# Optimization experiments

Measured on AMD Instinct MI355X. Metric: run time of the kernel, lower is better.

## Reference

```python
import jax, jax.numpy as jnp
import numpy as np

N = 100000
E = 1600000
IN = 256
H = 4
D = 32           # n_hidden per head
C = 47           # n_classes per head in last layer
NEG_SLOPE = 0.2


def setup_inputs() -> dict:
    key = jax.random.key(0)
    ks = jax.random.split(key, 20)
    x = jax.random.normal(ks[0], (N, IN), dtype=jnp.float32)
    src = jax.random.randint(ks[1], (E,), 0, N, dtype=jnp.int32)
    dst = jax.random.randint(ks[2], (E,), 0, N, dtype=jnp.int32)
    s = 0.05
    inp = {"x": x, "src": src, "dst": dst}
    # layer 0: in 256 -> (H=4, D=32)
    inp["W0s"] = jax.random.normal(ks[3], (IN, H * D), dtype=jnp.float32) * s
    inp["W0d"] = jax.random.normal(ks[4], (IN, H * D), dtype=jnp.float32) * s
    inp["a0l"] = jax.random.normal(ks[5], (H, D), dtype=jnp.float32) * s
    inp["a0r"] = jax.random.normal(ks[6], (H, D), dtype=jnp.float32) * s
    inp["b0"] = jnp.zeros((H, D), dtype=jnp.float32)
    # layer 1: in 128 -> (4, 32)
    inp["W1s"] = jax.random.normal(ks[7], (H * D, H * D), dtype=jnp.float32) * s
    inp["W1d"] = jax.random.normal(ks[8], (H * D, H * D), dtype=jnp.float32) * s
    inp["a1l"] = jax.random.normal(ks[9], (H, D), dtype=jnp.float32) * s
    inp["a1r"] = jax.random.normal(ks[10], (H, D), dtype=jnp.float32) * s
    inp["b1"] = jnp.zeros((H, D), dtype=jnp.float32)
    # layer 2: in 128 -> (4, 47), no activation
    inp["W2s"] = jax.random.normal(ks[11], (H * D, H * C), dtype=jnp.float32) * s
    inp["W2d"] = jax.random.normal(ks[12], (H * D, H * C), dtype=jnp.float32) * s
    inp["a2l"] = jax.random.normal(ks[13], (H, C), dtype=jnp.float32) * s
    inp["a2r"] = jax.random.normal(ks[14], (H, C), dtype=jnp.float32) * s
    inp["b2"] = jnp.zeros((H, C), dtype=jnp.float32)
    return inp


def _gat_layer(h, src, dst, Ws, Wd, al, ar, b):
    # h: [N, F_in]; full-graph block so h_dst == h
    n = h.shape[0]
    heads, dout = al.shape
    fs = (h @ Ws).reshape(n, heads, dout)   # [N, H, D]
    fd = (h @ Wd).reshape(n, heads, dout)
    el = jnp.sum(fs * al, axis=-1)          # [N, H]
    er = jnp.sum(fd * ar, axis=-1)
    e = el[src] + er[dst]                   # [E, H]
    e = jnp.where(e > 0, e, NEG_SLOPE * e)  # leaky_relu
    # segment softmax over incoming edges of each dst node
    m = jax.lax.stop_gradient(jax.ops.segment_max(e, dst, num_segments=n))
    ez = jnp.exp(e - m[dst])
    denom = jax.ops.segment_sum(ez, dst, num_segments=n)
    alpha = ez / denom[dst]                 # [E, H]
    msg = fs[src] * alpha[:, :, None]       # [E, H, D]
    rst = jax.ops.segment_sum(msg, dst, num_segments=n)  # [N, H, D]
    return rst + b


def reference(x, src, dst,
              W0s, W0d, a0l, a0r, b0,
              W1s, W1d, a1l, a1r, b1,
              W2s, W2d, a2l, a2r, b2):
    h = _gat_layer(x, src, dst, W0s, W0d, a0l, a0r, b0)
    h = jax.nn.relu(h).reshape(h.shape[0], -1)           # flatten(1)
    h = _gat_layer(h, src, dst, W1s, W1d, a1l, a1r, b1)
    h = jax.nn.relu(h).reshape(h.shape[0], -1)
    h = _gat_layer(h, src, dst, W2s, W2d, a2l, a2r, b2)  # [N, H, C]
    h = h.mean(axis=1)                                   # mean over heads
    return jax.nn.log_softmax(h, axis=-1)
```

## Files before the change

kernel.cpp:

```cpp
#include <hip/hip_runtime.h>
#include <math.h>

#define NEG_SLOPE 0.2f

typedef _Float16 half2v __attribute__((ext_vector_type(2)));
typedef _Float16 half8 __attribute__((ext_vector_type(8)));
typedef float float4v __attribute__((ext_vector_type(4)));
typedef float float2v __attribute__((ext_vector_type(2)));

__device__ __forceinline__ float lrelu(float x) { return x > 0.f ? x : NEG_SLOPE * x; }

__device__ __forceinline__ float sel4(const float4 v, int h) {
  float r = v.x;
  r = (h == 1) ? v.y : r;
  r = (h == 2) ? v.z : r;
  r = (h == 3) ? v.w : r;
  return r;
}

__device__ __forceinline__ unsigned char f32_to_fp8(float a) {
  int v = __builtin_amdgcn_cvt_pk_fp8_f32(a, 0.f, 0, false);
  return (unsigned char)(v & 0xff);
}

__device__ __forceinline__ void acc16(float2v acc[8], uint4 d, float ez) {
  float2v ez2 = {ez, ez};
  float2v c;
  c = __builtin_amdgcn_cvt_pk_f32_fp8((int)d.x, false); acc[0] += ez2 * c;
  c = __builtin_amdgcn_cvt_pk_f32_fp8((int)d.x, true);  acc[1] += ez2 * c;
  c = __builtin_amdgcn_cvt_pk_f32_fp8((int)d.y, false); acc[2] += ez2 * c;
  c = __builtin_amdgcn_cvt_pk_f32_fp8((int)d.y, true);  acc[3] += ez2 * c;
  c = __builtin_amdgcn_cvt_pk_f32_fp8((int)d.z, false); acc[4] += ez2 * c;
  c = __builtin_amdgcn_cvt_pk_f32_fp8((int)d.z, true);  acc[5] += ez2 * c;
  c = __builtin_amdgcn_cvt_pk_f32_fp8((int)d.w, false); acc[6] += ez2 * c;
  c = __builtin_amdgcn_cvt_pk_f32_fp8((int)d.w, true);  acc[7] += ez2 * c;
}


__global__ void k_hist(const int* __restrict__ dst, int* __restrict__ cnt, int E) {
  int i = blockIdx.x * blockDim.x + threadIdx.x;
  if (i < E) atomicAdd(&cnt[dst[i]], 1);
}

__global__ __launch_bounds__(256) void k_offsets(const int* __restrict__ cnt,
                                                 int* __restrict__ row_start,
                                                 int* __restrict__ gcount, int N) {
  __shared__ int s[256];
  __shared__ int base;
  int tid = threadIdx.x;
  int i = blockIdx.x * 256 + tid;
  int c = (i < N) ? cnt[i] : 0;
  s[tid] = c;
  __syncthreads();
  for (int off = 1; off < 256; off <<= 1) {
    int v = 0;
    if (tid >= off) v = s[tid - off];
    __syncthreads();
    if (tid >= off) s[tid] += v;
    __syncthreads();
  }
  if (tid == 255) base = atomicAdd(gcount, s[255]);
  __syncthreads();
  if (i < N) row_start[i] = base + s[tid] - c;
}

__global__ void k_scatter(const int* __restrict__ src, const int* __restrict__ dst,
                          const int* __restrict__ row_start, int* __restrict__ fill,
                          int* __restrict__ srcs, int E) {
  int i = blockIdx.x * blockDim.x + threadIdx.x;
  if (i < E) {
    int d = dst[i];
    int p = row_start[d] + atomicAdd(&fill[d], 1);
    srcs[p] = src[i];
  }
}

__device__ __forceinline__ void wlr_one(const float* Ws, const float* Wd,
                                        const float* al, const float* ar,
                                        float* wlr, int K, int Dh, int i) {
  int M = 4 * Dh;
  int k = i >> 2, h = i & 3;
  float sl = 0.f, sr = 0.f;
  for (int d = 0; d < Dh; d++) {
    sl += Ws[(size_t)k * M + h * Dh + d] * al[h * Dh + d];
    sr += Wd[(size_t)k * M + h * Dh + d] * ar[h * Dh + d];
  }
  wlr[k * 8 + h] = sl;
  wlr[k * 8 + 4 + h] = sr;
}

__global__ __launch_bounds__(256) void k_prep(
    const float* __restrict__ W0s, const float* __restrict__ W0d,
    const float* __restrict__ a0l, const float* __restrict__ a0r,
    const float* __restrict__ W1s, const float* __restrict__ W1d,
    const float* __restrict__ a1l, const float* __restrict__ a1r,
    const float* __restrict__ W2s, const float* __restrict__ W2d,
    const float* __restrict__ a2l, const float* __restrict__ a2r,
    float* __restrict__ wlr0, float* __restrict__ wlr1, float* __restrict__ wlr2,
    _Float16* __restrict__ Wt0, _Float16* __restrict__ Wt1, _Float16* __restrict__ Wt2) {
  int i = blockIdx.x * 256 + threadIdx.x;
  if (i < 1024) {
    wlr_one(W0s, W0d, a0l, a0r, wlr0, 256, 32, i);
  } else if (i < 1536) {
    wlr_one(W1s, W1d, a1l, a1r, wlr1, 128, 32, i - 1024);
  } else if (i < 2048) {
    wlr_one(W2s, W2d, a2l, a2r, wlr2, 128, 47, i - 1536);
  } else if (i < 2048 + 32768) {
    int j = i - 2048;
    int m = j >> 8, k = j & 255;
    Wt0[j] = (_Float16)W0s[(size_t)k * 128 + m];
  } else if (i < 2048 + 32768 + 16384) {
    int j = i - (2048 + 32768);
    int m = j >> 7, k = j & 127;
    Wt1[j] = (_Float16)W1s[(size_t)k * 128 + m];
  } else if (i < 2048 + 32768 + 16384 + 24576) {
    int j = i - (2048 + 32768 + 16384);
    int r = j >> 7, k = j & 127;
    int h = r / 48, c = r % 48;
    float v = (c < 47) ? W2s[(size_t)k * 188 + 47 * h + c] : 0.f;
    Wt2[j] = (_Float16)v;
  }
}

template <int BN, typename AT>
__global__ __launch_bounds__(256) void k_gemm_mfma(const AT* __restrict__ A,
                                                   const _Float16* __restrict__ Bt,
                                                   const float* __restrict__ wlr,
                                                   unsigned char* __restrict__ C,
                                                   float* __restrict__ el,
                                                   float* __restrict__ er, int N, int K) {
  constexpr int NT = BN / 64;
  constexpr int ASZ = 4 * 64 * 8;
  constexpr int BSZ = (BN / 16) * 64 * 8;
  constexpr int SSZ = ASZ + BSZ;
  __shared__ __align__(16) _Float16 smem[SSZ];
  __shared__ float swlr[2048];
  _Float16* As = smem;
  _Float16* Bs = smem + ASZ;

  const int tid = threadIdx.x;
  const int lane = tid & 63;
  const int w = tid >> 6;
  const int row0 = blockIdx.x * 64;

  for (int i = tid; i < K * 8; i += 256) swlr[i] = wlr[i];
  __syncthreads();

  float4v acc[4][NT];
#pragma unroll
  for (int i = 0; i < 4; i++)
#pragma unroll
    for (int j = 0; j < NT; j++) acc[i][j] = (float4v){0.f, 0.f, 0.f, 0.f};
  float p[8] = {0, 0, 0, 0, 0, 0, 0, 0};

  const int ar_ = tid >> 2, aq = tid & 3;
  for (int k0 = 0; k0 < K; k0 += 32) {
    {
      int gr = row0 + ar_;
      float a8[8];
      if (gr < N) {
        if constexpr (sizeof(AT) == 4) {
          const float4* pp = (const float4*)&A[(size_t)gr * K + k0 + aq * 8];
          float4 u0 = pp[0], u1 = pp[1];
          a8[0] = u0.x; a8[1] = u0.y; a8[2] = u0.z; a8[3] = u0.w;
          a8[4] = u1.x; a8[5] = u1.y; a8[6] = u1.z; a8[7] = u1.w;
        } else {
          half8 hv = *(const half8*)&A[(size_t)gr * K + k0 + aq * 8];
#pragma unroll
          for (int j = 0; j < 8; j++) a8[j] = (float)hv[j];
        }
      } else {
#pragma unroll
        for (int j = 0; j < 8; j++) a8[j] = 0.f;
      }
      half8 v;
#pragma unroll
      for (int j = 0; j < 8; j++) v[j] = (_Float16)a8[j];
      *(half8*)&As[(size_t)(((ar_ >> 4) * 64) + (ar_ & 15) + 16 * aq) * 8] = v;
#pragma unroll
      for (int j = 0; j < 8; j++) {
        const float av = a8[j];
        const float* wp = &swlr[(k0 + aq * 8 + j) * 8];
        float4 w0 = *(const float4*)wp;
        float4 w1 = *(const float4*)(wp + 4);
        p[0] += av * w0.x; p[1] += av * w0.y; p[2] += av * w0.z; p[3] += av * w0.w;
        p[4] += av * w1.x; p[5] += av * w1.y; p[6] += av * w1.z; p[7] += av * w1.w;
      }
    }
#pragma unroll
    for (int i = 0; i < NT; i++) {
      int idx = tid + i * 256;
      int n = idx >> 2, q = idx & 3;
      half8 v = *(const half8*)&Bt[(size_t)n * K + k0 + q * 8];
      *(half8*)&Bs[(size_t)((n >> 4) * 64 + (n & 15) + 16 * q) * 8] = v;
    }
    __syncthreads();
    half8 af[4];
#pragma unroll
    for (int mt = 0; mt < 4; mt++) af[mt] = *(half8*)&As[(size_t)(mt * 64 + lane) * 8];
#pragma unroll
    for (int nt = 0; nt < NT; nt++) {
      half8 bf = *(half8*)&Bs[(size_t)((w * NT + nt) * 64 + lane) * 8];
#pragma unroll
      for (int mt = 0; mt < 4; mt++)
        acc[mt][nt] = __builtin_amdgcn_mfma_f32_16x16x32_f16(af[mt], bf, acc[mt][nt], 0, 0, 0);
    }
    __syncthreads();
  }

#pragma unroll
  for (int j = 0; j < 8; j++) swlr[(ar_ * 4 + aq) * 8 + j] = p[j];

  unsigned char* cs = (unsigned char*)smem;
  const int quad = lane >> 4;
#pragma unroll
  for (int mt = 0; mt < 4; mt++)
#pragma unroll
    for (int nt = 0; nt < NT; nt++)
#pragma unroll
      for (int reg = 0; reg < 4; reg++) {
        int r = mt * 16 + quad * 4 + reg;
        int cc = (w * NT + nt) * 16 + (lane & 15);
        cs[r * BN + cc] = f32_to_fp8(acc[mt][nt][reg]);
      }
  __syncthreads();
  if (tid < 64) {
    int gr = row0 + tid;
    if (gr < N) {
      float e[8];
#pragma unroll
      for (int j = 0; j < 8; j++)
        e[j] = swlr[(tid * 4 + 0) * 8 + j] + swlr[(tid * 4 + 1) * 8 + j] +
               swlr[(tid * 4 + 2) * 8 + j] + swlr[(tid * 4 + 3) * 8 + j];
      *(float4*)&el[(size_t)gr * 4] = make_float4(e[0], e[1], e[2], e[3]);
      *(float4*)&er[(size_t)gr * 4] = make_float4(e[4], e[5], e[6], e[7]);
    }
  }
  constexpr int PER = (64 * BN) / (256 * 16);
  const uint4* s4 = (const uint4*)cs;
#pragma unroll
  for (int i = 0; i < PER; i++) {
    int idx = tid + i * 256;
    int r = idx / (BN / 16), c16 = idx % (BN / 16);
    int gr = row0 + r;
    if (gr < N) *(uint4*)&C[(size_t)gr * BN + c16 * 16] = s4[idx];
  }
}

__global__ __launch_bounds__(256) void k_edge_mid(
    const unsigned char* __restrict__ F, const float* __restrict__ el,
    const float* __restrict__ er, const int* __restrict__ row_start,
    const int* __restrict__ cnt, const int* __restrict__ srcs,
    const float* __restrict__ bias, _Float16* __restrict__ hout, int N) {
  __shared__ float sEz[4][64][4];
  __shared__ int sU[4][64];
  int lane = threadIdx.x & 63;
  int w = threadIdx.x >> 6;
  int v = blockIdx.x * 4 + w;
  if (v >= N) return;
  int start = row_start[v], deg = cnt[v];
  float4 erv = *(const float4*)&er[(size_t)v * 4];
  const int g8 = lane >> 3;
  const int sl = lane & 7;
  const int h = sl >> 1;
  float2v acc2[8];
#pragma unroll
  for (int i = 0; i < 8; i++) acc2[i] = (float2v){0.f, 0.f};
  float4 lsum = make_float4(0.f, 0.f, 0.f, 0.f);

  for (int c = 0; c < deg; c += 64) {
    int take = min(64, deg - c);
    if (lane < take) {
      int u = srcs[start + c + lane];
      float4 e = *(const float4*)&el[(size_t)u * 4];
      float4 ez;
      ez.x = __expf(lrelu(e.x + erv.x));
      ez.y = __expf(lrelu(e.y + erv.y));
      ez.z = __expf(lrelu(e.z + erv.z));
      ez.w = __expf(lrelu(e.w + erv.w));
      lsum.x += ez.x; lsum.y += ez.y; lsum.z += ez.z; lsum.w += ez.w;
      sU[w][lane] = u;
      *(float4*)&sEz[w][lane][0] = ez;
    }
    int kk = g8;
    if (kk < take) {
      int u0 = sU[w][kk];
      float ez0 = sEz[w][kk][h];
      uint4 d0 = *(const uint4*)&F[((unsigned)u0 << 7) + 16u * (unsigned)sl];
      for (kk += 8; kk < take; kk += 8) {
        int u1 = sU[w][kk];
        float ez1 = sEz[w][kk][h];
        uint4 d1 = *(const uint4*)&F[((unsigned)u1 << 7) + 16u * (unsigned)sl];
        acc16(acc2, d0, ez0);
        d0 = d1; ez0 = ez1;
      }
      acc16(acc2, d0, ez0);
    }
  }
#pragma unroll
  for (int m = 8; m < 64; m <<= 1)
#pragma unroll
    for (int i = 0; i < 8; i++) {
      acc2[i].x += __shfl_xor(acc2[i].x, m);
      acc2[i].y += __shfl_xor(acc2[i].y, m);
    }
#pragma unroll
  for (int msk = 1; msk < 64; msk <<= 1) {
    lsum.x += __shfl_xor(lsum.x, msk);
    lsum.y += __shfl_xor(lsum.y, msk);
    lsum.z += __shfl_xor(lsum.z, msk);
    lsum.w += __shfl_xor(lsum.w, msk);
  }
  if (g8 == 0) {
    float inv = (deg > 0) ? 1.f / sel4(lsum, h) : 0.f;
    const float4* bp = (const float4*)&bias[16 * sl];
    float4 b0v = bp[0], b1v = bp[1], b2v = bp[2], b3v = bp[3];
    float bb[16] = {b0v.x, b0v.y, b0v.z, b0v.w, b1v.x, b1v.y, b1v.z, b1v.w,
                    b2v.x, b2v.y, b2v.z, b2v.w, b3v.x, b3v.y, b3v.z, b3v.w};
    half8 o0, o1;
#pragma unroll
    for (int j = 0; j < 8; j++) {
      float a = acc2[j >> 1][j & 1];
      o0[j] = (_Float16)fmaxf(fmaf(a, inv, bb[j]), 0.f);
    }
#pragma unroll
    for (int j = 0; j < 8; j++) {
      float a = acc2[(j + 8) >> 1][j & 1];
      o1[j] = (_Float16)fmaxf(fmaf(a, inv, bb[j + 8]), 0.f);
    }
    *(half8*)&hout[(size_t)v * 128 + 16 * sl] = o0;
    *(half8*)&hout[(size_t)v * 128 + 16 * sl + 8] = o1;
  }
}

__global__ __launch_bounds__(256) void k_edge_final(
    const unsigned char* __restrict__ F, const float* __restrict__ el,
    const float* __restrict__ er, const int* __restrict__ row_start,
    const int* __restrict__ cnt, const int* __restrict__ srcs,
    const float* __restrict__ b2, float* __restrict__ out, int N) {
  __shared__ float sEz[4][64][4];
  __shared__ int sU[4][64];
  __shared__ float red[4][192];
  int lane = threadIdx.x & 63;
  int w = threadIdx.x >> 6;
  int v = blockIdx.x * 4 + w;
  if (v >= N) return;
  int start = row_start[v], deg = cnt[v];
  float4 erv = *(const float4*)&er[(size_t)v * 4];
  const int e0 = lane / 12;
  const int sl = lane - e0 * 12;
  const bool act = e0 < 5;
  const int h = sl / 3;
  float2v acc2[8];
#pragma unroll
  for (int i = 0; i < 8; i++) acc2[i] = (float2v){0.f, 0.f};
  float4 lsum = make_float4(0.f, 0.f, 0.f, 0.f);

  for (int c = 0; c < deg; c += 64) {
    int take = min(64, deg - c);
    if (lane < take) {
      int u = srcs[start + c + lane];
      float4 e = *(const float4*)&el[(size_t)u * 4];
      float4 ez;
      ez.x = __expf(lrelu(e.x + erv.x));
      ez.y = __expf(lrelu(e.y + erv.y));
      ez.z = __expf(lrelu(e.z + erv.z));
      ez.w = __expf(lrelu(e.w + erv.w));
      lsum.x += ez.x; lsum.y += ez.y; lsum.z += ez.z; lsum.w += ez.w;
      sU[w][lane] = u;
      *(float4*)&sEz[w][lane][0] = ez;
    }
    if (act) {
      int kk = e0;
      if (kk < take) {
        int u0 = sU[w][kk];
        float ez0 = sEz[w][kk][h];
        uint4 d0 = *(const uint4*)&F[(unsigned)u0 * 192u + 16u * (unsigned)sl];
        for (kk += 5; kk < take; kk += 5) {
          int u1 = sU[w][kk];
          float ez1 = sEz[w][kk][h];
          uint4 d1 = *(const uint4*)&F[(unsigned)u1 * 192u + 16u * (unsigned)sl];
          acc16(acc2, d0, ez0);
          d0 = d1; ez0 = ez1;
        }
        acc16(acc2, d0, ez0);
      }
    }
  }
#pragma unroll
  for (int i = 0; i < 8; i++) {
    float ax = acc2[i].x, ay = acc2[i].y;
    float t1x = ax + __shfl(ax, lane + 12);
    float t1y = ay + __shfl(ay, lane + 12);
    float t2x = t1x + __shfl(t1x, lane + 24);
    float t2y = t1y + __shfl(t1y, lane + 24);
    acc2[i].x = t2x + __shfl(ax, lane + 48);
    acc2[i].y = t2y + __shfl(ay, lane + 48);
  }
#pragma unroll
  for (int msk = 1; msk < 64; msk <<= 1) {
    lsum.x += __shfl_xor(lsum.x, msk);
    lsum.y += __shfl_xor(lsum.y, msk);
    lsum.z += __shfl_xor(lsum.z, msk);
    lsum.w += __shfl_xor(lsum.w, msk);
  }
  if (lane < 12) {
    float inv = (deg > 0) ? 1.f / sel4(lsum, h) : 0.f;
#pragma unroll
    for (int j = 0; j < 8; j++) {
      red[w][sl * 16 + 2 * j] = acc2[j].x * inv;
      red[w][sl * 16 + 2 * j + 1] = acc2[j].y * inv;
    }
  }
  float g = -INFINITY;
  if (lane < 47) {
    float s4 = red[w][lane] + red[w][lane + 48] + red[w][lane + 96] + red[w][lane + 144];
    float bsum = b2[lane] + b2[47 + lane] + b2[94 + lane] + b2[141 + lane];
    g = 0.25f * (s4 + bsum);
  }
  float gm = g;
#pragma unroll
  for (int msk = 1; msk < 64; msk <<= 1) gm = fmaxf(gm, __shfl_xor(gm, msk));
  float ex = (lane < 47) ? __expf(g - gm) : 0.f;
  float s = ex;
#pragma unroll
  for (int msk = 1; msk < 64; msk <<= 1) s += __shfl_xor(s, msk);
  if (lane < 47) out[(size_t)v * 47 + lane] = g - gm - __logf(s);
}

extern "C" void kernel_launch(void* const* d_in, const int* in_sizes, int n_in,
                              void* d_out, int out_size, void* d_ws, size_t ws_size,
                              hipStream_t stream) {
  const float* x = (const float*)d_in[0];
  const int* src = (const int*)d_in[1];
  const int* dst = (const int*)d_in[2];
  const float* W0s = (const float*)d_in[3];
  const float* W0d = (const float*)d_in[4];
  const float* a0l = (const float*)d_in[5];
  const float* a0r = (const float*)d_in[6];
  const float* b0 = (const float*)d_in[7];
  const float* W1s = (const float*)d_in[8];
  const float* W1d = (const float*)d_in[9];
  const float* a1l = (const float*)d_in[10];
  const float* a1r = (const float*)d_in[11];
  const float* b1 = (const float*)d_in[12];
  const float* W2s = (const float*)d_in[13];
  const float* W2d = (const float*)d_in[14];
  const float* a2l = (const float*)d_in[15];
  const float* a2r = (const float*)d_in[16];
  const float* b2 = (const float*)d_in[17];
  float* out = (float*)d_out;

  const int N = in_sizes[0] / 256;
  const int E = in_sizes[1];

  char* w = (char*)d_ws;
  size_t off = 0;
  auto alloc = [&](size_t bytes) -> void* {
    void* p = w + off;
    off += (bytes + 255) & ~(size_t)255;
    return p;
  };
  int* gcount = (int*)alloc(4);
  int* cnt = (int*)alloc((size_t)N * 4);
  int* fill = (int*)alloc((size_t)N * 4);
  size_t zbytes = off;
  int* row_start = (int*)alloc((size_t)N * 4);
  int* srcs = (int*)alloc((size_t)E * 4);
  float* wlr0 = (float*)alloc(256 * 8 * 4);
  float* wlr1 = (float*)alloc(128 * 8 * 4);
  float* wlr2 = (float*)alloc(128 * 8 * 4);
  _Float16* Wt0 = (_Float16*)alloc(128 * 256 * 2);
  _Float16* Wt1 = (_Float16*)alloc(128 * 128 * 2);
  _Float16* Wt2 = (_Float16*)alloc(192 * 128 * 2);
  float* el = (float*)alloc((size_t)N * 4 * 4);
  float* er = (float*)alloc((size_t)N * 4 * 4);
  unsigned char* F = (unsigned char*)alloc((size_t)N * 192);
  _Float16* Ha = (_Float16*)alloc((size_t)N * 128 * 2);
  _Float16* Hc = (_Float16*)alloc((size_t)N * 128 * 2);
  (void)ws_size;

  hipMemsetAsync(d_ws, 0, zbytes, stream);
  k_hist<<<(E + 255) / 256, 256, 0, stream>>>(dst, cnt, E);
  k_offsets<<<(N + 255) / 256, 256, 0, stream>>>(cnt, row_start, gcount, N);
  k_scatter<<<(E + 255) / 256, 256, 0, stream>>>(src, dst, row_start, fill, srcs, E);
  k_prep<<<(75776 + 255) / 256, 256, 0, stream>>>(W0s, W0d, a0l, a0r, W1s, W1d, a1l, a1r,
                                                  W2s, W2d, a2l, a2r, wlr0, wlr1, wlr2,
                                                  Wt0, Wt1, Wt2);

  int gemm_grid = (N + 63) / 64;
  int node_grid = (N + 3) / 4;

  k_gemm_mfma<128, float><<<gemm_grid, 256, 0, stream>>>(x, Wt0, wlr0, F, el, er, N, 256);
  k_edge_mid<<<node_grid, 256, 0, stream>>>(F, el, er, row_start, cnt, srcs, b0, Ha, N);

  k_gemm_mfma<128, _Float16><<<gemm_grid, 256, 0, stream>>>(Ha, Wt1, wlr1, F, el, er, N, 128);
  k_edge_mid<<<node_grid, 256, 0, stream>>>(F, el, er, row_start, cnt, srcs, b1, Hc, N);

  k_gemm_mfma<192, _Float16><<<gemm_grid, 256, 0, stream>>>(Hc, Wt2, wlr2, F, el, er, N, 128);
  k_edge_final<<<node_grid, 256, 0, stream>>>(F, el, er, row_start, cnt, srcs, b2, out, N);
}
```

Baseline: 712.8 us.

## Split edge aggregation across feature slices and separate final log-softmax combine

The edge aggregation kernels now split each node's feature row into slices handled by different blocks: two 64-byte halves for the middle layers and three slices for the final layer. Each lane covers fewer bytes, so 16 edges are processed in parallel instead of 8 or 5. Block indices are interleaved so that slices of nearby nodes run close together, which is meant to improve gather parallelism and keep the shared source rows in cache. The final layer writes per-slice partial results in fp16 to a scratch buffer, and a new combine kernel then does the head mean and log-softmax. In exchange, edge indices and attention exponentials are recomputed for every slice, and the extra kernel adds a launch and a scratch-buffer round trip.

```diff
diff --git a/kernel.cpp b/kernel.cpp
--- a/kernel.cpp
+++ b/kernel.cpp
@@ -247,22 +247,114 @@
   }
 }
 
-__global__ __launch_bounds__(256) void k_edge_mid(
+__global__ __launch_bounds__(256) void k_edge_mid_x(
     const unsigned char* __restrict__ F, const float* __restrict__ el,
     const float* __restrict__ er, const int* __restrict__ row_start,
     const int* __restrict__ cnt, const int* __restrict__ srcs,
     const float* __restrict__ bias, _Float16* __restrict__ hout, int N) {
+  __shared__ float sEz[4][64][2];
+  __shared__ int sU[4][64];
+  const int NB = (N + 3) >> 2;
+  const int p = blockIdx.x & 7;
+  const int s = p >> 2;
+  const int nb = (blockIdx.x >> 3) * 4 + (p & 3);
+  if (nb >= NB) return;
+  const int lane = threadIdx.x & 63;
+  const int w = threadIdx.x >> 6;
+  const int v = nb * 4 + w;
+  if (v >= N) return;
+  const int start = row_start[v], deg = cnt[v];
+  const float2 erv = *(const float2*)&er[(size_t)v * 4 + 2 * s];
+  const int g = lane >> 2;
+  const int sl = lane & 3;
+  const int hl = sl >> 1;
+  float2v acc2[8];
+#pragma unroll
+  for (int i = 0; i < 8; i++) acc2[i] = (float2v){0.f, 0.f};
+  float2 lsum = make_float2(0.f, 0.f);
+
+  for (int c = 0; c < deg; c += 64) {
+    int take = min(64, deg - c);
+    if (lane < take) {
+      int u = srcs[start + c + lane];
+      float2 e = *(const float2*)&el[(size_t)u * 4 + 2 * s];
+      float ezx = __expf(lrelu(e.x + erv.x));
+      float ezy = __expf(lrelu(e.y + erv.y));
+      lsum.x += ezx; lsum.y += ezy;
+      sU[w][lane] = u;
+      sEz[w][lane][0] = ezx;
+      sEz[w][lane][1] = ezy;
+    }
+    int kk = g;
+    if (kk < take) {
+      int u0 = sU[w][kk];
+      float ez0 = sEz[w][kk][hl];
+      uint4 d0 = *(const uint4*)&F[((unsigned)u0 << 7) + (unsigned)(s * 64 + sl * 16)];
+      for (kk += 16; kk < take; kk += 16) {
+        int u1 = sU[w][kk];
+        float ez1 = sEz[w][kk][hl];
+        uint4 d1 = *(const uint4*)&F[((unsigned)u1 << 7) + (unsigned)(s * 64 + sl * 16)];
+        acc16(acc2, d0, ez0);
+        d0 = d1; ez0 = ez1;
+      }
+      acc16(acc2, d0, ez0);
+    }
+  }
+#pragma unroll
+  for (int m = 4; m < 64; m <<= 1)
+#pragma unroll
+    for (int i = 0; i < 8; i++) {
+      acc2[i].x += __shfl_xor(acc2[i].x, m);
+      acc2[i].y += __shfl_xor(acc2[i].y, m);
+    }
+#pragma unroll
+  for (int msk = 1; msk < 64; msk <<= 1) {
+    lsum.x += __shfl_xor(lsum.x, msk);
+    lsum.y += __shfl_xor(lsum.y, msk);
+  }
+  if (g == 0) {
+    float inv = (deg > 0) ? 1.f / (hl ? lsum.y : lsum.x) : 0.f;
+    const int f0 = s * 64 + sl * 16;
+    const float4* bp = (const float4*)&bias[f0];
+    float4 b0v = bp[0], b1v = bp[1], b2v = bp[2], b3v = bp[3];
+    float bb[16] = {b0v.x, b0v.y, b0v.z, b0v.w, b1v.x, b1v.y, b1v.z, b1v.w,
+                    b2v.x, b2v.y, b2v.z, b2v.w, b3v.x, b3v.y, b3v.z, b3v.w};
+    half8 o0, o1;
+#pragma unroll
+    for (int j = 0; j < 8; j++)
+      o0[j] = (_Float16)fmaxf(fmaf(acc2[j >> 1][j & 1], inv, bb[j]), 0.f);
+#pragma unroll
+    for (int j = 0; j < 8; j++)
+      o1[j] = (_Float16)fmaxf(fmaf(acc2[(j + 8) >> 1][j & 1], inv, bb[j + 8]), 0.f);
+    *(half8*)&hout[(size_t)v * 128 + f0] = o0;
+    *(half8*)&hout[(size_t)v * 128 + f0 + 8] = o1;
+  }
+}
+
+__global__ __launch_bounds__(256) void k_edge_final_x(
+    const unsigned char* __restrict__ F, const float* __restrict__ el,
+    const float* __restrict__ er, const int* __restrict__ row_start,
+    const int* __restrict__ cnt, const int* __restrict__ srcs,
+    _Float16* __restrict__ Pf, int N) {
   __shared__ float sEz[4][64][4];
   __shared__ int sU[4][64];
-  int lane = threadIdx.x & 63;
-  int w = threadIdx.x >> 6;
-  int v = blockIdx.x * 4 + w;
+  const int NB = (N + 3) >> 2;
+  const int p = blockIdx.x & 7;
+  const int s = (p < 3) ? 0 : ((p < 6) ? 1 : 2);
+  const int r = p - 3 * s;
+  const int K = (s == 2) ? 2 : 3;
+  const int nb = (blockIdx.x >> 3) * K + r;
+  if (nb >= NB) return;
+  const int lane = threadIdx.x & 63;
+  const int w = threadIdx.x >> 6;
+  const int v = nb * 4 + w;
   if (v >= N) return;
-  int start = row_start[v], deg = cnt[v];
-  float4 erv = *(const float4*)&er[(size_t)v * 4];
-  const int g8 = lane >> 3;
-  const int sl = lane & 7;
-  const int h = sl >> 1;
+  const int start = row_start[v], deg = cnt[v];
+  const float4 erv = *(const float4*)&er[(size_t)v * 4];
+  const int g = lane >> 2;
+  const int sl = lane & 3;
+  const int k16 = 4 * s + sl;
+  const int h = k16 / 3;
   float2v acc2[8];
 #pragma unroll
   for (int i = 0; i < 8; i++) acc2[i] = (float2v){0.f, 0.f};
@@ -282,15 +374,15 @@
       sU[w][lane] = u;
       *(float4*)&sEz[w][lane][0] = ez;
     }
-    int kk = g8;
+    int kk = g;
     if (kk < take) {
       int u0 = sU[w][kk];
       float ez0 = sEz[w][kk][h];
-      uint4 d0 = *(const uint4*)&F[((unsigned)u0 << 7) + 16u * (unsigned)sl];
-      for (kk += 8; kk < take; kk += 8) {
+      uint4 d0 = *(const uint4*)&F[(unsigned)u0 * 192u + (unsigned)(k16 * 16)];
+      for (kk += 16; kk < take; kk += 16) {
         int u1 = sU[w][kk];
         float ez1 = sEz[w][kk][h];
-        uint4 d1 = *(const uint4*)&F[((unsigned)u1 << 7) + 16u * (unsigned)sl];
+        uint4 d1 = *(const uint4*)&F[(unsigned)u1 * 192u + (unsigned)(k16 * 16)];
         acc16(acc2, d0, ez0);
         d0 = d1; ez0 = ez1;
       }
@@ -298,7 +390,7 @@
     }
   }
 #pragma unroll
-  for (int m = 8; m < 64; m <<= 1)
+  for (int m = 4; m < 64; m <<= 1)
 #pragma unroll
     for (int i = 0; i < 8; i++) {
       acc2[i].x += __shfl_xor(acc2[i].x, m);
@@ -311,121 +403,41 @@
     lsum.z += __shfl_xor(lsum.z, msk);
     lsum.w += __shfl_xor(lsum.w, msk);
   }
-  if (g8 == 0) {
+  if (g == 0) {
     float inv = (deg > 0) ? 1.f / sel4(lsum, h) : 0.f;
-    const float4* bp = (const float4*)&bias[16 * sl];
-    float4 b0v = bp[0], b1v = bp[1], b2v = bp[2], b3v = bp[3];
-    float bb[16] = {b0v.x, b0v.y, b0v.z, b0v.w, b1v.x, b1v.y, b1v.z, b1v.w,
-                    b2v.x, b2v.y, b2v.z, b2v.w, b3v.x, b3v.y, b3v.z, b3v.w};
     half8 o0, o1;
 #pragma unroll
-    for (int j = 0; j < 8; j++) {
-      float a = acc2[j >> 1][j & 1];
-      o0[j] = (_Float16)fmaxf(fmaf(a, inv, bb[j]), 0.f);
-    }
-#pragma unroll
-    for (int j = 0; j < 8; j++) {
-      float a = acc2[(j + 8) >> 1][j & 1];
-      o1[j] = (_Float16)fmaxf(fmaf(a, inv, bb[j + 8]), 0.f);
-    }
-    *(half8*)&hout[(size_t)v * 128 + 16 * sl] = o0;
-    *(half8*)&hout[(size_t)v * 128 + 16 * sl + 8] = o1;
-  }
-}
-
-__global__ __launch_bounds__(256) void k_edge_final(
-    const unsigned char* __restrict__ F, const float* __restrict__ el,
-    const float* __restrict__ er, const int* __restrict__ row_start,
-    const int* __restrict__ cnt, const int* __restrict__ srcs,
-    const float* __restrict__ b2, float* __restrict__ out, int N) {
-  __shared__ float sEz[4][64][4];
-  __shared__ int sU[4][64];
-  __shared__ float red[4][192];
+    for (int j = 0; j < 8; j++) o0[j] = (_Float16)(acc2[j >> 1][j & 1] * inv);
+#pragma unroll
+    for (int j = 0; j < 8; j++) o1[j] = (_Float16)(acc2[(j + 8) >> 1][j & 1] * inv);
+    *(half8*)&Pf[(size_t)v * 192 + k16 * 16] = o0;
+    *(half8*)&Pf[(size_t)v * 192 + k16 * 16 + 8] = o1;
+  }
+}
+
+__global__ __launch_bounds__(256) void k_comb(const _Float16* __restrict__ Pf,
+                                              const float* __restrict__ b2,
+                                              float* __restrict__ out, int N) {
   int lane = threadIdx.x & 63;
   int w = threadIdx.x >> 6;
   int v = blockIdx.x * 4 + w;
   if (v >= N) return;
-  int start = row_start[v], deg = cnt[v];
-  float4 erv = *(const float4*)&er[(size_t)v * 4];
-  const int e0 = lane / 12;
-  const int sl = lane - e0 * 12;
-  const bool act = e0 < 5;
-  const int h = sl / 3;
-  float2v acc2[8];
-#pragma unroll
-  for (int i = 0; i < 8; i++) acc2[i] = (float2v){0.f, 0.f};
-  float4 lsum = make_float4(0.f, 0.f, 0.f, 0.f);
-
-  for (int c = 0; c < deg; c += 64) {
-    int take = min(64, deg - c);
-    if (lane < take) {
-      int u = srcs[start + c + lane];
-      float4 e = *(const float4*)&el[(size_t)u * 4];
-      float4 ez;
-      ez.x = __expf(lrelu(e.x + erv.x));
-      ez.y = __expf(lrelu(e.y + erv.y));
-      ez.z = __expf(lrelu(e.z + erv.z));
-      ez.w = __expf(lrelu(e.w + erv.w));
-      lsum.x += ez.x; lsum.y += ez.y; lsum.z += ez.z; lsum.w += ez.w;
-      sU[w][lane] = u;
-      *(float4*)&sEz[w][lane][0] = ez;
-    }
-    if (act) {
-      int kk = e0;
-      if (kk < take) {
-        int u0 = sU[w][kk];
-        float ez0 = sEz[w][kk][h];
-        uint4 d0 = *(const uint4*)&F[(unsigned)u0 * 192u + 16u * (unsigned)sl];
-        for (kk += 5; kk < take; kk += 5) {
-          int u1 = sU[w][kk];
-          float ez1 = sEz[w][kk][h];
-          uint4 d1 = *(const uint4*)&F[(unsigned)u1 * 192u + 16u * (unsigned)sl];
-          acc16(acc2, d0, ez0);
-          d0 = d1; ez0 = ez1;
-        }
-        acc16(acc2, d0, ez0);
-      }
-    }
-  }
-#pragma unroll
-  for (int i = 0; i < 8; i++) {
-    float ax = acc2[i].x, ay = acc2[i].y;
-    float t1x = ax + __shfl(ax, lane + 12);
-    float t1y = ay + __shfl(ay, lane + 12);
-    float t2x = t1x + __shfl(t1x, lane + 24);
-    float t2y = t1y + __shfl(t1y, lane + 24);
-    acc2[i].x = t2x + __shfl(ax, lane + 48);
-    acc2[i].y = t2y + __shfl(ay, lane + 48);
-  }
-#pragma unroll
-  for (int msk = 1; msk < 64; msk <<= 1) {
-    lsum.x += __shfl_xor(lsum.x, msk);
-    lsum.y += __shfl_xor(lsum.y, msk);
-    lsum.z += __shfl_xor(lsum.z, msk);
-    lsum.w += __shfl_xor(lsum.w, msk);
-  }
-  if (lane < 12) {
-    float inv = (deg > 0) ? 1.f / sel4(lsum, h) : 0.f;
-#pragma unroll
-    for (int j = 0; j < 8; j++) {
-      red[w][sl * 16 + 2 * j] = acc2[j].x * inv;
-      red[w][sl * 16 + 2 * j + 1] = acc2[j].y * inv;
-    }
-  }
-  float g = -INFINITY;
+  float gv = -INFINITY;
   if (lane < 47) {
-    float s4 = red[w][lane] + red[w][lane + 48] + red[w][lane + 96] + red[w][lane + 144];
-    float bsum = b2[lane] + b2[47 + lane] + b2[94 + lane] + b2[141 + lane];
-    g = 0.25f * (s4 + bsum);
-  }
-  float gm = g;
+    const _Float16* pr = &Pf[(size_t)v * 192];
+    float s4 = (float)pr[lane] + (float)pr[lane + 48] + (float)pr[lane + 96] +
+               (float)pr[lane + 144];
+    float bs = b2[lane] + b2[47 + lane] + b2[94 + lane] + b2[141 + lane];
+    gv = 0.25f * (s4 + bs);
+  }
+  float gm = gv;
 #pragma unroll
   for (int msk = 1; msk < 64; msk <<= 1) gm = fmaxf(gm, __shfl_xor(gm, msk));
-  float ex = (lane < 47) ? __expf(g - gm) : 0.f;
-  float s = ex;
-#pragma unroll
-  for (int msk = 1; msk < 64; msk <<= 1) s += __shfl_xor(s, msk);
-  if (lane < 47) out[(size_t)v * 47 + lane] = g - gm - __logf(s);
+  float ex = (lane < 47) ? __expf(gv - gm) : 0.f;
+  float ss = ex;
+#pragma unroll
+  for (int msk = 1; msk < 64; msk <<= 1) ss += __shfl_xor(ss, msk);
+  if (lane < 47) out[(size_t)v * 47 + lane] = gv - gm - __logf(ss);
 }
 
 extern "C" void kernel_launch(void* const* d_in, const int* in_sizes, int n_in,
@@ -478,6 +490,7 @@
   unsigned char* F = (unsigned char*)alloc((size_t)N * 192);
   _Float16* Ha = (_Float16*)alloc((size_t)N * 128 * 2);
   _Float16* Hc = (_Float16*)alloc((size_t)N * 128 * 2);
+  _Float16* Pf = Ha;
   (void)ws_size;
 
   hipMemsetAsync(d_ws, 0, zbytes, stream);
@@ -488,15 +501,18 @@
                                                   W2s, W2d, a2l, a2r, wlr0, wlr1, wlr2,
                                                   Wt0, Wt1, Wt2);
 
-  int gemm_grid = (N + 63) / 64;
-  int node_grid = (N + 3) / 4;
+  const int NB = (N + 3) / 4;
+  const int gemm_grid = (N + 63) / 64;
+  const int grid_mid = ((2 * NB + 7) / 8) * 8;
+  const int grid_fin = 8 * ((NB + 1) / 2);
 
   k_gemm_mfma<128, float><<<gemm_grid, 256, 0, stream>>>(x, Wt0, wlr0, F, el, er, N, 256);
-  k_edge_mid<<<node_grid, 256, 0, stream>>>(F, el, er, row_start, cnt, srcs, b0, Ha, N);
+  k_edge_mid_x<<<grid_mid, 256, 0, stream>>>(F, el, er, row_start, cnt, srcs, b0, Ha, N);
 
   k_gemm_mfma<128, _Float16><<<gemm_grid, 256, 0, stream>>>(Ha, Wt1, wlr1, F, el, er, N, 128);
-  k_edge_mid<<<node_grid, 256, 0, stream>>>(F, el, er, row_start, cnt, srcs, b1, Hc, N);
+  k_edge_mid_x<<<grid_mid, 256, 0, stream>>>(F, el, er, row_start, cnt, srcs, b1, Hc, N);
 
   k_gemm_mfma<192, _Float16><<<gemm_grid, 256, 0, stream>>>(Hc, Wt2, wlr2, F, el, er, N, 128);
-  k_edge_final<<<node_grid, 256, 0, stream>>>(F, el, er, row_start, cnt, srcs, b2, out, N);
-}
+  k_edge_final_x<<<grid_fin, 256, 0, stream>>>(F, el, er, row_start, cnt, srcs, Pf, N);
+  k_comb<<<(N + 3) / 4, 256, 0, stream>>>(Pf, b2, out, N);
+}
```

Measured after the change: 1.147 ms. 60.9% more time.
